# Kernel tuning notes

Measured on AMD Instinct MI355X. Metric: run time of the kernel, lower is better.

## Reference

```python
import jax, jax.numpy as jnp
import numpy as np

N_HEADS = 16

def setup_inputs() -> dict:
    key = jax.random.key(0)
    k1, k2, k3 = jax.random.split(key, 3)
    B, T, C = 4, 2048, 1024
    x = jax.random.normal(k1, (B, T, C), dtype=jnp.float32)
    w_qkv = jax.random.normal(k2, (C, 3 * C), dtype=jnp.float32) * (1.0 / np.sqrt(C))
    w_out = jax.random.normal(k3, (C, C), dtype=jnp.float32) * (1.0 / np.sqrt(C))
    return {"x": x, "w_qkv": w_qkv, "w_out": w_out}

def reference(x, w_qkv, w_out):
    B, T, C = x.shape
    H = N_HEADS
    D = C // H
    qkv = jnp.einsum('btc,cf->btf', x, w_qkv).reshape(B, T, 3, H, D)
    q, k, v = qkv[:, :, 0], qkv[:, :, 1], qkv[:, :, 2]  # [B,T,H,D]
    q = q.transpose(0, 2, 1, 3)  # [B,H,T,D]
    k = k.transpose(0, 2, 1, 3)
    v = v.transpose(0, 2, 1, 3)
    scale = 1.0 / jnp.sqrt(jnp.asarray(D, dtype=x.dtype))
    scores = jnp.einsum('bhqd,bhkd->bhqk', q, k) * scale  # [B,H,T,T]
    causal = jnp.tril(jnp.ones((T, T), dtype=bool))
    scores = jnp.where(causal[None, None], scores, jnp.asarray(-jnp.inf, dtype=scores.dtype))
    attn = jax.nn.softmax(scores, axis=-1)
    ctx = jnp.einsum('bhqk,bhkd->bhqd', attn, v)  # [B,H,T,D]
    ctx = ctx.transpose(0, 2, 1, 3).reshape(B, T, C)
    return jnp.einsum('btc,co->bto', ctx, w_out)
```

## Files before the change

### kernel.cpp

```cpp
#include <hip/hip_runtime.h>

typedef __attribute__((ext_vector_type(8))) short bf16x8;
typedef __attribute__((ext_vector_type(4))) float f32x4;
typedef __attribute__((ext_vector_type(4))) unsigned short u16x4;

#define MFMA16(a, b, c) __builtin_amdgcn_mfma_f32_16x16x32_bf16((a), (b), (c), 0, 0, 0)

__device__ __forceinline__ unsigned short f2bf(float f) {
    union { float f; unsigned int u; } x; x.f = f;
    unsigned int r = x.u + 0x7FFFu + ((x.u >> 16) & 1u);
    return (unsigned short)(r >> 16);
}
__device__ __forceinline__ float bf2f(unsigned short h) {
    union { unsigned int u; float f; } x; x.u = ((unsigned int)h) << 16;
    return x.f;
}
__device__ __forceinline__ void gload_lds16(const void* g, void* l) {
    __builtin_amdgcn_global_load_lds(
        (const __attribute__((address_space(1))) unsigned int*)g,
        (__attribute__((address_space(3))) unsigned int*)l,
        16, 0, 0);
}

__global__ void cast_x(const float* __restrict__ in, unsigned short* __restrict__ hi,
                       int n) {
    int i = (blockIdx.x * blockDim.x + threadIdx.x) * 4;
    if (i >= n) return;
    float4 v = *(const float4*)(in + i);
    float vv[4] = {v.x, v.y, v.z, v.w};
    u16x4 h;
#pragma unroll
    for (int j = 0; j < 4; ++j) h[j] = f2bf(vv[j]);
    *(u16x4*)(hi + i) = h;
}

__global__ void tcast_k(const float* __restrict__ in, unsigned short* __restrict__ out,
                        int K, int N) {
    __shared__ float tile[64][65];
    int n0 = blockIdx.x * 64, k0 = blockIdx.y * 64;
    for (int i = threadIdx.x; i < 4096; i += 256) {
        int r = i >> 6, c = i & 63;
        tile[r][c] = in[(size_t)(k0 + r) * N + n0 + c];
    }
    __syncthreads();
    for (int i = threadIdx.x; i < 4096; i += 256) {
        int r = i >> 6, c = i & 63;
        out[(size_t)(n0 + r) * K + k0 + c] = f2bf(tile[c][r]);
    }
}

__global__ __launch_bounds__(256, 2) void gemm_qkv(
    const unsigned short* __restrict__ A,
    const unsigned short* __restrict__ Bt,
    unsigned short* __restrict__ qout, unsigned short* __restrict__ kout,
    unsigned short* __restrict__ vtout) {
    const int K = 1024;
    __shared__ __align__(16) unsigned short sA[4096], sB[4096];
    int tid = threadIdx.x, lane = tid & 63, w = tid >> 6;
    int c = lane & 15, quad = lane >> 4;
    int wm = (w >> 1) * 64, wn = (w & 1) * 64;
    int m0 = blockIdx.y * 128, n0 = blockIdx.x * 128;

    f32x4 acc[4][4];
#pragma unroll
    for (int i = 0; i < 4; i++)
#pragma unroll
        for (int j = 0; j < 4; j++) acc[i][j] = (f32x4){0.f, 0.f, 0.f, 0.f};

    int c0 = tid, c1 = 256 + tid;
    int r0 = c0 >> 2, kc0 = (c0 & 3) * 8;
    int r1 = c1 >> 2, kc1 = (c1 & 3) * 8;

    for (int kk = 0; kk < K; kk += 32) {
        gload_lds16(A + (size_t)(m0 + r0) * K + kk + kc0, &sA[c0 * 8]);
        gload_lds16(A + (size_t)(m0 + r1) * K + kk + kc1, &sA[c1 * 8]);
        gload_lds16(Bt + (size_t)(n0 + r0) * K + kk + kc0, &sB[c0 * 8]);
        gload_lds16(Bt + (size_t)(n0 + r1) * K + kk + kc1, &sB[c1 * 8]);
        __syncthreads();
        bf16x8 af[4], bfr[4];
#pragma unroll
        for (int mt = 0; mt < 4; ++mt)
            af[mt] = *(const bf16x8*)&sA[(wm + mt * 16 + c) * 32 + quad * 8];
#pragma unroll
        for (int nt = 0; nt < 4; ++nt)
            bfr[nt] = *(const bf16x8*)&sB[(wn + nt * 16 + c) * 32 + quad * 8];
#pragma unroll
        for (int mt = 0; mt < 4; ++mt)
#pragma unroll
            for (int nt = 0; nt < 4; ++nt)
                acc[mt][nt] = MFMA16(af[mt], bfr[nt], acc[mt][nt]);
        __syncthreads();
    }

    const float QSCALE = 0.1803368801111601f;
#pragma unroll
    for (int mt = 0; mt < 4; ++mt) {
#pragma unroll
        for (int nt = 0; nt < 4; ++nt) {
#pragma unroll
            for (int r = 0; r < 4; ++r) {
                int row = m0 + wm + mt * 16 + quad * 4 + r;
                int col = n0 + wn + nt * 16 + c;
                float v = acc[mt][nt][r];
                int which = col >> 10;
                int h = (col >> 6) & 15;
                int d = col & 63;
                int b = row >> 11;
                int t = row & 2047;
                size_t bh_ = (size_t)(b * 16 + h);
                if (which == 0)
                    qout[(bh_ * 2048 + t) * 64 + d] = f2bf(v * QSCALE);
                else if (which == 1)
                    kout[(bh_ * 2048 + t) * 64 + d] = f2bf(v);
                else
                    vtout[(bh_ * 64 + d) * 2048 + t] = f2bf(v);
            }
        }
    }
}

__global__ __launch_bounds__(256, 2) void gemm2_bt(
    const unsigned short* __restrict__ A,
    const unsigned short* __restrict__ Bt,
    float* __restrict__ out) {
    const int K = 1024, N = 1024;
    __shared__ __align__(16) unsigned short sA[4096], sB[4096];
    int tid = threadIdx.x, lane = tid & 63, w = tid >> 6;
    int c = lane & 15, quad = lane >> 4;
    int wm = (w >> 1) * 64, wn = (w & 1) * 64;
    int m0 = blockIdx.y * 128, n0 = blockIdx.x * 128;

    f32x4 acc[4][4];
#pragma unroll
    for (int i = 0; i < 4; i++)
#pragma unroll
        for (int j = 0; j < 4; j++) acc[i][j] = (f32x4){0.f, 0.f, 0.f, 0.f};

    int c0 = tid, c1 = 256 + tid;
    int r0 = c0 >> 2, kc0 = (c0 & 3) * 8;
    int r1 = c1 >> 2, kc1 = (c1 & 3) * 8;

    for (int kk = 0; kk < K; kk += 32) {
        gload_lds16(A + (size_t)(m0 + r0) * K + kk + kc0, &sA[c0 * 8]);
        gload_lds16(A + (size_t)(m0 + r1) * K + kk + kc1, &sA[c1 * 8]);
        gload_lds16(Bt + (size_t)(n0 + r0) * K + kk + kc0, &sB[c0 * 8]);
        gload_lds16(Bt + (size_t)(n0 + r1) * K + kk + kc1, &sB[c1 * 8]);
        __syncthreads();
        bf16x8 af[4], bfr[4];
#pragma unroll
        for (int mt = 0; mt < 4; ++mt)
            af[mt] = *(const bf16x8*)&sA[(wm + mt * 16 + c) * 32 + quad * 8];
#pragma unroll
        for (int nt = 0; nt < 4; ++nt)
            bfr[nt] = *(const bf16x8*)&sB[(wn + nt * 16 + c) * 32 + quad * 8];
#pragma unroll
        for (int mt = 0; mt < 4; ++mt)
#pragma unroll
            for (int nt = 0; nt < 4; ++nt)
                acc[mt][nt] = MFMA16(af[mt], bfr[nt], acc[mt][nt]);
        __syncthreads();
    }

#pragma unroll
    for (int mt = 0; mt < 4; ++mt)
#pragma unroll
        for (int nt = 0; nt < 4; ++nt)
#pragma unroll
            for (int r = 0; r < 4; ++r) {
                int row = m0 + wm + mt * 16 + quad * 4 + r;
                int col = n0 + wn + nt * 16 + c;
                out[(size_t)row * N + col] = acc[mt][nt][r];
            }
}

#define SSTR 72
__global__ __launch_bounds__(256, 2) void attn_k(
    const unsigned short* __restrict__ q,
    const unsigned short* __restrict__ k,
    const unsigned short* __restrict__ vt,
    unsigned short* __restrict__ ctx) {
    const int T = 2048, D = 64;
    __shared__ __align__(16) unsigned short sK[2][64 * SSTR];
    __shared__ __align__(16) unsigned short sV[2][64 * SSTR];
    __shared__ __align__(16) unsigned short sP[4][32 * SSTR];

    int tid = threadIdx.x, lane = tid & 63, w = tid >> 6;
    int c = lane & 15, quad = lane >> 4;
    int pair = blockIdx.x, bh = blockIdx.y;

    const unsigned short* qh = q + (size_t)bh * T * D;
    const unsigned short* kh = k + (size_t)bh * T * D;
    const unsigned short* vh = vt + (size_t)bh * D * T;
    unsigned short* sPw = sP[w];
    int b = bh >> 4, hh = bh & 15;

    int dv = tid >> 3, tcv = (tid & 7) * 8;

    for (int half = 0; half < 2; ++half) {
        int jt = half ? (15 - pair) : pair;
        int q0 = jt * 128;
        int nkt = 2 * jt + 2;
        int qrow[2] = {q0 + w * 16 + c, q0 + 64 + w * 16 + c};

        bf16x8 bq[2][2];
#pragma unroll
        for (int g = 0; g < 2; ++g) {
            bq[g][0] = *(const bf16x8*)&qh[(size_t)qrow[g] * D + quad * 8];
            bq[g][1] = *(const bf16x8*)&qh[(size_t)qrow[g] * D + 32 + quad * 8];
        }

        f32x4 o[2][4];
#pragma unroll
        for (int g = 0; g < 2; ++g)
#pragma unroll
            for (int mt = 0; mt < 4; ++mt) o[g][mt] = (f32x4){0.f, 0.f, 0.f, 0.f};
        float m_i[2] = {-1.0e30f, -1.0e30f}, l_i[2] = {0.f, 0.f};

        bf16x8 kr0 = *(const bf16x8*)&kh[(size_t)lane * D + w * 8];
        bf16x8 kr1 = *(const bf16x8*)&kh[(size_t)lane * D + w * 8 + 32];
        bf16x8 vr0 = *(const bf16x8*)&vh[(size_t)dv * T + tcv];
        bf16x8 vr1 = *(const bf16x8*)&vh[(size_t)(dv + 32) * T + tcv];
        __syncthreads();
        *(bf16x8*)&sK[0][lane * SSTR + w * 8] = kr0;
        *(bf16x8*)&sK[0][lane * SSTR + w * 8 + 32] = kr1;
        *(bf16x8*)&sV[0][dv * SSTR + tcv] = vr0;
        *(bf16x8*)&sV[0][(dv + 32) * SSTR + tcv] = vr1;
        __syncthreads();

        for (int kt = 0; kt < nkt; ++kt) {
            int cur = kt & 1;
            int kb = kt * 64;
            if (kt + 1 < nkt) {
                int kb2 = (kt + 1) * 64;
                kr0 = *(const bf16x8*)&kh[(size_t)(kb2 + lane) * D + w * 8];
                kr1 = *(const bf16x8*)&kh[(size_t)(kb2 + lane) * D + w * 8 + 32];
                vr0 = *(const bf16x8*)&vh[(size_t)dv * T + kb2 + tcv];
                vr1 = *(const bf16x8*)&vh[(size_t)(dv + 32) * T + kb2 + tcv];
            }
            const unsigned short* sKc = sK[cur];
            const unsigned short* sVc = sV[cur];

            bf16x8 ak0[4], ak1[4];
#pragma unroll
            for (int mt = 0; mt < 4; ++mt) {
                ak0[mt] = *(const bf16x8*)&sKc[(mt * 16 + c) * SSTR + quad * 8];
                ak1[mt] = *(const bf16x8*)&sKc[(mt * 16 + c) * SSTR + 32 + quad * 8];
            }

#pragma unroll
            for (int g = 0; g < 2; ++g) {
                f32x4 st[4];
#pragma unroll
                for (int mt = 0; mt < 4; ++mt) {
                    f32x4 z = (f32x4){0.f, 0.f, 0.f, 0.f};
                    z = MFMA16(ak0[mt], bq[g][0], z);
                    z = MFMA16(ak1[mt], bq[g][1], z);
                    st[mt] = z;
                }
                int qr = qrow[g];
                if (kb + 63 > qr) {
#pragma unroll
                    for (int mt = 0; mt < 4; ++mt)
#pragma unroll
                        for (int r = 0; r < 4; ++r)
                            if (kb + mt * 16 + quad * 4 + r > qr) st[mt][r] = -1.0e30f;
                }
                float vmax = fmaxf(
                    fmaxf(fmaxf(fmaxf(st[0][0], st[0][1]), fmaxf(st[0][2], st[0][3])),
                          fmaxf(fmaxf(st[1][0], st[1][1]), fmaxf(st[1][2], st[1][3]))),
                    fmaxf(fmaxf(fmaxf(st[2][0], st[2][1]), fmaxf(st[2][2], st[2][3])),
                          fmaxf(fmaxf(st[3][0], st[3][1]), fmaxf(st[3][2], st[3][3]))));
                vmax = fmaxf(vmax, __shfl_xor(vmax, 16));
                vmax = fmaxf(vmax, __shfl_xor(vmax, 32));
                float mnew = fmaxf(m_i[g], vmax);
                float alpha = __builtin_exp2f(m_i[g] - mnew);
                float rs = 0.f;
#pragma unroll
                for (int mt = 0; mt < 4; ++mt) {
                    u16x4 pb;
#pragma unroll
                    for (int r = 0; r < 4; ++r) {
                        float p = __builtin_exp2f(st[mt][r] - mnew);
                        unsigned short pw = f2bf(p);
                        rs += bf2f(pw);
                        pb[r] = pw;
                    }
                    *(u16x4*)&sPw[(g * 16 + c) * SSTR + mt * 16 + quad * 4] = pb;
                }
                rs += __shfl_xor(rs, 16);
                rs += __shfl_xor(rs, 32);
                l_i[g] = l_i[g] * alpha + rs;
                m_i[g] = mnew;
#pragma unroll
                for (int mt = 0; mt < 4; ++mt)
#pragma unroll
                    for (int r = 0; r < 4; ++r) o[g][mt][r] *= alpha;
            }

#pragma unroll
            for (int ch = 0; ch < 2; ++ch) {
                bf16x8 av[4];
#pragma unroll
                for (int mt = 0; mt < 4; ++mt)
                    av[mt] = *(const bf16x8*)&sVc[(mt * 16 + c) * SSTR + ch * 32 + quad * 8];
#pragma unroll
                for (int g = 0; g < 2; ++g) {
                    bf16x8 bp = *(const bf16x8*)&sPw[(g * 16 + c) * SSTR + ch * 32 + quad * 8];
#pragma unroll
                    for (int mt = 0; mt < 4; ++mt)
                        o[g][mt] = MFMA16(av[mt], bp, o[g][mt]);
                }
            }

            if (kt + 1 < nkt) {
                unsigned short* sKn = sK[1 - cur];
                unsigned short* sVn = sV[1 - cur];
                *(bf16x8*)&sKn[lane * SSTR + w * 8] = kr0;
                *(bf16x8*)&sKn[lane * SSTR + w * 8 + 32] = kr1;
                *(bf16x8*)&sVn[dv * SSTR + tcv] = vr0;
                *(bf16x8*)&sVn[(dv + 32) * SSTR + tcv] = vr1;
                __syncthreads();
            }
        }

#pragma unroll
        for (int g = 0; g < 2; ++g) {
            float inv = 1.0f / l_i[g];
#pragma unroll
            for (int mt = 0; mt < 4; ++mt) {
                u16x4 ob;
#pragma unroll
                for (int r = 0; r < 4; ++r) ob[r] = f2bf(o[g][mt][r] * inv);
                *(u16x4*)&ctx[(size_t)(b * T + qrow[g]) * 1024 + hh * 64 + mt * 16 + quad * 4] = ob;
            }
        }
    }
}

extern "C" void kernel_launch(void* const* d_in, const int* in_sizes, int n_in,
                              void* d_out, int out_size, void* d_ws, size_t ws_size,
                              hipStream_t stream) {
    const float* x     = (const float*)d_in[0];
    const float* w_qkv = (const float*)d_in[1];
    const float* w_out = (const float*)d_in[2];
    float* out = (float*)d_out;

    char* ws = (char*)d_ws;
    unsigned short* wqkvt = (unsigned short*)(ws + 0);
    unsigned short* woutt = (unsigned short*)(ws + 6291456);
    unsigned short* x_bf  = (unsigned short*)(ws + 8388608);
    unsigned short* qb    = (unsigned short*)(ws + 25165824);
    unsigned short* kb    = (unsigned short*)(ws + 41943040);
    unsigned short* vtb   = (unsigned short*)(ws + 58720256);
    unsigned short* ctx   = (unsigned short*)(ws + 8388608);

    cast_x<<<8192, 256, 0, stream>>>(x, x_bf, 8388608);
    tcast_k<<<dim3(48, 16), 256, 0, stream>>>(w_qkv, wqkvt, 1024, 3072);
    tcast_k<<<dim3(16, 16), 256, 0, stream>>>(w_out, woutt, 1024, 1024);
    gemm_qkv<<<dim3(24, 64), 256, 0, stream>>>(x_bf, wqkvt, qb, kb, vtb);
    attn_k<<<dim3(8, 64), 256, 0, stream>>>(qb, kb, vtb, ctx);
    gemm2_bt<<<dim3(8, 64), 256, 0, stream>>>(ctx, woutt, out);
}
```

Baseline: 314.0 us.

## Widen attention blocks to 512 threads with 256-row query tiles and cheaper P packing

```diff
diff --git a/kernel.cpp b/kernel.cpp
--- a/kernel.cpp
+++ b/kernel.cpp
@@ -11,9 +11,9 @@
     unsigned int r = x.u + 0x7FFFu + ((x.u >> 16) & 1u);
     return (unsigned short)(r >> 16);
 }
-__device__ __forceinline__ float bf2f(unsigned short h) {
-    union { unsigned int u; float f; } x; x.u = ((unsigned int)h) << 16;
-    return x.f;
+__device__ __forceinline__ unsigned int fbits(float f) {
+    union { float f; unsigned int u; } x; x.f = f;
+    return x.u;
 }
 __device__ __forceinline__ void gload_lds16(const void* g, void* l) {
     __builtin_amdgcn_global_load_lds(
@@ -174,7 +174,7 @@
 }
 
 #define SSTR 72
-__global__ __launch_bounds__(256, 2) void attn_k(
+__global__ __launch_bounds__(512, 4) void attn_k(
     const unsigned short* __restrict__ q,
     const unsigned short* __restrict__ k,
     const unsigned short* __restrict__ vt,
@@ -182,7 +182,7 @@
     const int T = 2048, D = 64;
     __shared__ __align__(16) unsigned short sK[2][64 * SSTR];
     __shared__ __align__(16) unsigned short sV[2][64 * SSTR];
-    __shared__ __align__(16) unsigned short sP[4][32 * SSTR];
+    __shared__ __align__(16) unsigned short sP[8][32 * SSTR];
 
     int tid = threadIdx.x, lane = tid & 63, w = tid >> 6;
     int c = lane & 15, quad = lane >> 4;
@@ -194,13 +194,15 @@
     unsigned short* sPw = sP[w];
     int b = bh >> 4, hh = bh & 15;
 
-    int dv = tid >> 3, tcv = (tid & 7) * 8;
+    int sr = tid >> 3, sc = (tid & 7) * 8;
 
     for (int half = 0; half < 2; ++half) {
-        int jt = half ? (15 - pair) : pair;
-        int q0 = jt * 128;
-        int nkt = 2 * jt + 2;
-        int qrow[2] = {q0 + w * 16 + c, q0 + 64 + w * 16 + c};
+        int jt = half ? (7 - pair) : pair;
+        int q0 = jt * 256;
+        int nkt = 4 * jt + 4;
+        int qrow[2];
+        qrow[0] = q0 + (w * 2) * 16 + c;
+        qrow[1] = qrow[0] + 16;
 
         bf16x8 bq[2][2];
 #pragma unroll
@@ -216,15 +218,11 @@
             for (int mt = 0; mt < 4; ++mt) o[g][mt] = (f32x4){0.f, 0.f, 0.f, 0.f};
         float m_i[2] = {-1.0e30f, -1.0e30f}, l_i[2] = {0.f, 0.f};
 
-        bf16x8 kr0 = *(const bf16x8*)&kh[(size_t)lane * D + w * 8];
-        bf16x8 kr1 = *(const bf16x8*)&kh[(size_t)lane * D + w * 8 + 32];
-        bf16x8 vr0 = *(const bf16x8*)&vh[(size_t)dv * T + tcv];
-        bf16x8 vr1 = *(const bf16x8*)&vh[(size_t)(dv + 32) * T + tcv];
-        __syncthreads();
-        *(bf16x8*)&sK[0][lane * SSTR + w * 8] = kr0;
-        *(bf16x8*)&sK[0][lane * SSTR + w * 8 + 32] = kr1;
-        *(bf16x8*)&sV[0][dv * SSTR + tcv] = vr0;
-        *(bf16x8*)&sV[0][(dv + 32) * SSTR + tcv] = vr1;
+        bf16x8 kr = *(const bf16x8*)&kh[(size_t)sr * D + sc];
+        bf16x8 vr = *(const bf16x8*)&vh[(size_t)sr * T + sc];
+        __syncthreads();
+        *(bf16x8*)&sK[0][sr * SSTR + sc] = kr;
+        *(bf16x8*)&sV[0][sr * SSTR + sc] = vr;
         __syncthreads();
 
         for (int kt = 0; kt < nkt; ++kt) {
@@ -232,10 +230,8 @@
             int kb = kt * 64;
             if (kt + 1 < nkt) {
                 int kb2 = (kt + 1) * 64;
-                kr0 = *(const bf16x8*)&kh[(size_t)(kb2 + lane) * D + w * 8];
-                kr1 = *(const bf16x8*)&kh[(size_t)(kb2 + lane) * D + w * 8 + 32];
-                vr0 = *(const bf16x8*)&vh[(size_t)dv * T + kb2 + tcv];
-                vr1 = *(const bf16x8*)&vh[(size_t)(dv + 32) * T + kb2 + tcv];
+                kr = *(const bf16x8*)&kh[(size_t)(kb2 + sr) * D + sc];
+                vr = *(const bf16x8*)&vh[(size_t)sr * T + kb2 + sc];
             }
             const unsigned short* sKc = sK[cur];
             const unsigned short* sVc = sV[cur];
@@ -277,15 +273,17 @@
                 float rs = 0.f;
 #pragma unroll
                 for (int mt = 0; mt < 4; ++mt) {
-                    u16x4 pb;
-#pragma unroll
-                    for (int r = 0; r < 4; ++r) {
-                        float p = __builtin_exp2f(st[mt][r] - mnew);
-                        unsigned short pw = f2bf(p);
-                        rs += bf2f(pw);
-                        pb[r] = pw;
-                    }
-                    *(u16x4*)&sPw[(g * 16 + c) * SSTR + mt * 16 + quad * 4] = pb;
+                    float p0 = __builtin_exp2f(st[mt][0] - mnew);
+                    float p1 = __builtin_exp2f(st[mt][1] - mnew);
+                    float p2 = __builtin_exp2f(st[mt][2] - mnew);
+                    float p3 = __builtin_exp2f(st[mt][3] - mnew);
+                    rs += (p0 + p1) + (p2 + p3);
+                    unsigned int w0 = __builtin_amdgcn_perm(
+                        fbits(p1) + 0x8000u, fbits(p0) + 0x8000u, 0x07060302u);
+                    unsigned int w1 = __builtin_amdgcn_perm(
+                        fbits(p3) + 0x8000u, fbits(p2) + 0x8000u, 0x07060302u);
+                    uint2 pk; pk.x = w0; pk.y = w1;
+                    *(uint2*)&sPw[(g * 16 + c) * SSTR + mt * 16 + quad * 4] = pk;
                 }
                 rs += __shfl_xor(rs, 16);
                 rs += __shfl_xor(rs, 32);
@@ -313,12 +311,8 @@
             }
 
             if (kt + 1 < nkt) {
-                unsigned short* sKn = sK[1 - cur];
-                unsigned short* sVn = sV[1 - cur];
-                *(bf16x8*)&sKn[lane * SSTR + w * 8] = kr0;
-                *(bf16x8*)&sKn[lane * SSTR + w * 8 + 32] = kr1;
-                *(bf16x8*)&sVn[dv * SSTR + tcv] = vr0;
-                *(bf16x8*)&sVn[(dv + 32) * SSTR + tcv] = vr1;
+                *(bf16x8*)&sK[1 - cur][sr * SSTR + sc] = kr;
+                *(bf16x8*)&sV[1 - cur][sr * SSTR + sc] = vr;
                 __syncthreads();
             }
         }
@@ -358,6 +352,6 @@
     tcast_k<<<dim3(48, 16), 256, 0, stream>>>(w_qkv, wqkvt, 1024, 3072);
     tcast_k<<<dim3(16, 16), 256, 0, stream>>>(w_out, woutt, 1024, 1024);
     gemm_qkv<<<dim3(24, 64), 256, 0, stream>>>(x_bf, wqkvt, qb, kb, vtb);
-    attn_k<<<dim3(8, 64), 256, 0, stream>>>(qb, kb, vtb, ctx);
+    attn_k<<<dim3(4, 64), 512, 0, stream>>>(qb, kb, vtb, ctx);
     gemm2_bt<<<dim3(8, 64), 256, 0, stream>>>(ctx, woutt, out);
 }
```

Result: slower. 335.1 us (+6.7%).
